# Kernel tuning notes

Hardware: AMD Instinct MI355X
Metric: run time of the kernel (lower is better)

Reference implementation:

```python
import jax, jax.numpy as jnp
import numpy as np

D = 1024
H = 16
HD = D // H
MLP = 4 * D
EPS = 1e-6
SCALE = HD ** -0.5


def _p(key, shape, s=0.02):
    return jax.random.normal(key, shape, dtype=jnp.float32) * s


def setup_inputs() -> dict:
    key = jax.random.key(0)
    ks = jax.random.split(key, 24)
    B, N, S = 4, 1024, 77
    return {
        "x": jax.random.normal(ks[0], (B, N, D), dtype=jnp.float32),
        "t_emb": jax.random.normal(ks[1], (B, D), dtype=jnp.float32),
        "context": jax.random.normal(ks[2], (B, S, D), dtype=jnp.float32),
        # AdaLN modulation: SiLU -> Linear(D, 6D)
        "adaln_w": _p(ks[3], (D, 6 * D)),
        "adaln_b": _p(ks[4], (6 * D,)),
        # self-attention
        "qkv_w": _p(ks[5], (D, 3 * D)),
        "qkv_b": _p(ks[6], (3 * D,)),
        "sa_proj_w": _p(ks[7], (D, D)),
        "sa_proj_b": _p(ks[8], (D,)),
        # cross-attention
        "q_w": _p(ks[9], (D, D)),
        "q_b": _p(ks[10], (D,)),
        "kv_w": _p(ks[11], (D, 2 * D)),
        "kv_b": _p(ks[12], (2 * D,)),
        "ca_proj_w": _p(ks[13], (D, D)),
        "ca_proj_b": _p(ks[14], (D,)),
        # MLP (GELU tanh)
        "fc1_w": _p(ks[15], (D, MLP)),
        "fc1_b": _p(ks[16], (MLP,)),
        "fc2_w": _p(ks[17], (MLP, D)),
        "fc2_b": _p(ks[18], (D,)),
    }


def _ln(x):
    # LayerNorm, elementwise_affine=False, eps=1e-6
    mu = jnp.mean(x, axis=-1, keepdims=True)
    var = jnp.var(x, axis=-1, keepdims=True)
    return (x - mu) * jax.lax.rsqrt(var + EPS)


def _heads(t):
    # [B, L, D] -> [B, H, L, HD]
    B, L, _ = t.shape
    return t.reshape(B, L, H, HD).transpose(0, 2, 1, 3)


def _attend(q, k, v):
    # q: [B,H,N,HD], k/v: [B,H,S,HD]
    attn = jnp.einsum("bhnd,bhsd->bhns", q, k) * SCALE
    attn = jax.nn.softmax(attn, axis=-1)
    o = jnp.einsum("bhns,bhsd->bhnd", attn, v)
    B, _, N, _ = q.shape
    return o.transpose(0, 2, 1, 3).reshape(B, N, D)


def reference(x, t_emb, context,
              adaln_w, adaln_b,
              qkv_w, qkv_b, sa_proj_w, sa_proj_b,
              q_w, q_b, kv_w, kv_b, ca_proj_w, ca_proj_b,
              fc1_w, fc1_b, fc2_w, fc2_b):
    B, N, _ = x.shape
    S = context.shape[1]

    # AdaLN modulation params
    mod = jax.nn.silu(t_emb) @ adaln_w + adaln_b            # [B, 6D]
    sh_sa, sc_sa, g_sa, sh_ff, sc_ff, g_ff = jnp.split(mod[:, None, :], 6, axis=-1)

    # --- self-attention branch ---
    xm = _ln(x) * (1.0 + sc_sa) + sh_sa
    qkv = (xm @ qkv_w + qkv_b).reshape(B, N, 3, H, HD)
    q = qkv[:, :, 0].transpose(0, 2, 1, 3)
    k = qkv[:, :, 1].transpose(0, 2, 1, 3)
    v = qkv[:, :, 2].transpose(0, 2, 1, 3)
    x_sa = _attend(q, k, v) @ sa_proj_w + sa_proj_b
    x = x + g_sa * x_sa

    # --- cross-attention branch ---
    xn = _ln(x)
    q = _heads(xn @ q_w + q_b)
    kv = (context @ kv_w + kv_b).reshape(B, S, 2, H, HD)
    k = kv[:, :, 0].transpose(0, 2, 1, 3)
    v = kv[:, :, 1].transpose(0, 2, 1, 3)
    x_ca = _attend(q, k, v) @ ca_proj_w + ca_proj_b
    x = x + x_ca

    # --- MLP branch ---
    xm = _ln(x) * (1.0 + sc_ff) + sh_ff
    h = jax.nn.gelu(xm @ fc1_w + fc1_b, approximate=True)
    x_ff = h @ fc2_w + fc2_b
    x = x + g_ff * x_ff
    return x
```

## Files before the change

kernel.cpp:

```cpp
#include <hip/hip_runtime.h>
#include <hip/hip_bf16.h>


#define D_MODEL 1024
#define NHEAD   16
#define HDIM    64
#define SEQ_N   1024
#define SEQ_S   77
#define BATCH   4
#define MLP_DIM 4096
#define ATT_SCALE 0.125f

typedef _Float16 f16;
typedef f16   f16x8 __attribute__((ext_vector_type(8)));
typedef float f32x4 __attribute__((ext_vector_type(4)));

__device__ __forceinline__ void gload16(const void* g, void* l) {
  __builtin_amdgcn_global_load_lds(
      (const __attribute__((address_space(1))) void*)g,
      (__attribute__((address_space(3))) void*)l, 16, 0, 0);
}

__global__ __launch_bounds__(256) void wt_kernel(
    const float* __restrict__ W, f16* __restrict__ Wt, int K, int N)
{
  __shared__ f16 tile[64][72];
  const int t = threadIdx.x;
  const int k0 = blockIdx.y * 64, n0 = blockIdx.x * 64;
  const int kr = t >> 4, nc = (t & 15) * 4;
#pragma unroll
  for (int p = 0; p < 4; ++p) {
    f32x4 v = *(const f32x4*)&W[(size_t)(k0 + kr + p * 16) * N + n0 + nc];
#pragma unroll
    for (int j = 0; j < 4; ++j) tile[nc + j][kr + p * 16] = (f16)v[j];
  }
  __syncthreads();
  const int nr = t >> 2, ck = (t & 3) * 16;
  *(f16x8*)&Wt[(size_t)(n0 + nr) * K + k0 + ck]     = *(const f16x8*)&tile[nr][ck];
  *(f16x8*)&Wt[(size_t)(n0 + nr) * K + k0 + ck + 8] = *(const f16x8*)&tile[nr][ck + 8];
}

__global__ __launch_bounds__(256) void mod_kernel(
    const float* __restrict__ t_emb, const float* __restrict__ w,
    const float* __restrict__ bias, float* __restrict__ mod)
{
  __shared__ float s[D_MODEL];
  const int b = blockIdx.y;
  for (int i = threadIdx.x; i < D_MODEL; i += 256) {
    float v = t_emb[b * D_MODEL + i];
    s[i] = v / (1.f + expf(-v));
  }
  __syncthreads();
  const int col = blockIdx.x * 256 + threadIdx.x;
  float acc = 0.f;
  for (int k = 0; k < D_MODEL; ++k) acc += s[k] * w[(size_t)k * (6 * D_MODEL) + col];
  mod[(size_t)b * (6 * D_MODEL) + col] = acc + bias[col];
}

__global__ __launch_bounds__(256) void init_x_kernel(
    const float* __restrict__ x, float* __restrict__ X, int n)
{
  int i = blockIdx.x * 256 + threadIdx.x;
  if (i < n) X[i] = x[i];
}

__global__ __launch_bounds__(256) void cvt_kernel(
    const float* __restrict__ in, f16* __restrict__ out, int n)
{
  int i = blockIdx.x * 256 + threadIdx.x;
  if (i < n) out[i] = (f16)in[i];
}

__global__ __launch_bounds__(256) void lnmod_kernel(
    const float* __restrict__ X, const float* __restrict__ mod,
    int scale_off, int shift_off, f16* __restrict__ out)
{
  const int row = blockIdx.x;
  const int b = row >> 10;
  const float* xr = X + (size_t)row * D_MODEL;
  float s = 0.f, s2 = 0.f;
  for (int i = threadIdx.x; i < D_MODEL; i += 256) {
    float v = xr[i]; s += v; s2 += v * v;
  }
  const int lane = threadIdx.x & 63, w = threadIdx.x >> 6;
  for (int o = 32; o; o >>= 1) { s += __shfl_xor(s, o); s2 += __shfl_xor(s2, o); }
  __shared__ float rs[4], rs2[4];
  if (lane == 0) { rs[w] = s; rs2[w] = s2; }
  __syncthreads();
  s = rs[0] + rs[1] + rs[2] + rs[3];
  s2 = rs2[0] + rs2[1] + rs2[2] + rs2[3];
  const float mean = s * (1.f / D_MODEL);
  const float var = s2 * (1.f / D_MODEL) - mean * mean;
  const float rstd = rsqrtf(var + 1e-6f);
  const float* mrow = mod ? mod + (size_t)b * (6 * D_MODEL) : nullptr;
  for (int i = threadIdx.x; i < D_MODEL; i += 256) {
    float v = (xr[i] - mean) * rstd;
    if (mrow) v = v * (1.f + mrow[scale_off + i]) + mrow[shift_off + i];
    out[(size_t)row * D_MODEL + i] = (f16)v;
  }
}

template <int BN>
__global__ __launch_bounds__(256) void gemm_kernel(
    const f16* __restrict__ A, const f16* __restrict__ Wt,
    const float* __restrict__ bias,
    float* __restrict__ Xres, const float* __restrict__ gate,
    f16* __restrict__ outb, float* __restrict__ outf,
    int M, int N, int K, int do_gelu)
{
  constexpr int NB = BN / 32;
  __shared__ f16 As[3][128 * 32];
  __shared__ f16 Bs[3][BN * 32];
  const int t = threadIdx.x;
  const int lane = t & 63, wave = t >> 6;
  const int wr = wave >> 1, wc = wave & 1;
  int bx = blockIdx.x, by = blockIdx.y;
  {
    const int gx = gridDim.x;
    const int nwg = gx * gridDim.y;
    if ((nwg & 7) == 0) {
      int wg = by * gx + bx;
      wg = (wg & 7) * (nwg >> 3) + (wg >> 3);
      bx = wg % gx; by = wg / gx;
    }
  }
  const int brow = by * 128, bcol = bx * BN;
  const int fr = lane & 15, fq = lane >> 4;
  const int sr = t >> 2, sc = (t & 3) * 8;
  const int ldsoff = wave * 512;

  f32x4 acc[4][NB] = {};
  const f16* Ag = A  + (size_t)(brow + sr) * K + sc;
  const f16* Bg = Wt + (size_t)(bcol + sr) * K + sc;
  const int nt = K >> 5;

  auto STAGE = [&](int buf, int k0) {
    gload16(Ag + k0,                  &As[buf][ldsoff]);
    gload16(Ag + (size_t)64 * K + k0, &As[buf][2048 + ldsoff]);
    gload16(Bg + k0,                  &Bs[buf][ldsoff]);
    if constexpr (BN == 128)
      gload16(Bg + (size_t)64 * K + k0, &Bs[buf][2048 + ldsoff]);
  };

  STAGE(0, 0);
  if (nt > 1) STAGE(1, 32);
  int cur = 0;
  for (int kt = 0; kt < nt; ++kt) {
    if constexpr (BN == 128)
      asm volatile("s_waitcnt vmcnt(4)\n\ts_barrier" ::: "memory");
    else
      asm volatile("s_waitcnt vmcnt(3)\n\ts_barrier" ::: "memory");
    int nx = cur + 2; if (nx >= 3) nx -= 3;
    if (kt + 2 < nt) STAGE(nx, (kt + 2) * 32);
    f16x8 af[4], bf[NB];
#pragma unroll
    for (int m = 0; m < 4; ++m)
      af[m] = *(const f16x8*)&As[cur][(wr * 64 + m * 16 + fr) * 32 + fq * 8];
#pragma unroll
    for (int n = 0; n < NB; ++n)
      bf[n] = *(const f16x8*)&Bs[cur][(wc * (BN / 2) + n * 16 + fr) * 32 + fq * 8];
#pragma unroll
    for (int m = 0; m < 4; ++m)
#pragma unroll
      for (int n = 0; n < NB; ++n)
        acc[m][n] = __builtin_amdgcn_mfma_f32_16x16x32_f16(af[m], bf[n], acc[m][n], 0, 0, 0);
    ++cur; if (cur == 3) cur = 0;
  }

#pragma unroll
  for (int m = 0; m < 4; ++m) {
#pragma unroll
    for (int n = 0; n < NB; ++n) {
      const int col = bcol + wc * (BN / 2) + n * 16 + fr;
      const int row0 = brow + wr * 64 + m * 16 + fq * 4;
      const float bv = bias ? bias[col] : 0.f;
#pragma unroll
      for (int r = 0; r < 4; ++r) {
        const int row = row0 + r;
        if (row >= M) continue;
        float v = acc[m][n][r] + bv;
        if (do_gelu) {
          float u = v;
          v = 0.5f * u * (1.f + tanhf(0.7978845608028654f * (u + 0.044715f * u * u * u)));
        }
        if (Xres) {
          const float g = gate ? gate[(size_t)(row >> 10) * (6 * D_MODEL) + col] : 1.0f;
          v = Xres[(size_t)row * N + col] + g * v;
          Xres[(size_t)row * N + col] = v;
        }
        if (outb) outb[(size_t)row * N + col] = (f16)v;
        if (outf) outf[(size_t)row * N + col] = v;
      }
    }
  }
}

__global__ __launch_bounds__(256) void sa_attn_kernel(
    const f16* __restrict__ qkv, f16* __restrict__ out)
{
  const int qt = blockIdx.x, h = blockIdx.y, b = blockIdx.z;
  __shared__ f16 Kl[64][72];
  __shared__ f16 Vt[64][72];
  __shared__ f16 Pl[4][16][72];
  const int t = threadIdx.x;
  const int lane = t & 63, w = t >> 6;
  const int fr = lane & 15, fq = lane >> 4;
  const size_t base = (size_t)b * SEQ_N * 3072 + h * 64;

  const int qrow = qt * 64 + w * 16 + fr;
  f16x8 qa[2];
#pragma unroll
  for (int kk = 0; kk < 2; ++kk)
    qa[kk] = *(const f16x8*)&qkv[base + (size_t)qrow * 3072 + kk * 32 + fq * 8];

  f32x4 o_acc[4] = {};
  float m_run[4], l_run[4];
#pragma unroll
  for (int r = 0; r < 4; ++r) { m_run[r] = -1e30f; l_run[r] = 0.f; }

  const int sr = t >> 2, scol = (t & 3) * 8;
  for (int s0 = 0; s0 < SEQ_N; s0 += 64) {
    __syncthreads();
#pragma unroll
    for (int p = 0; p < 2; ++p) {
      *(f16x8*)&Kl[sr][scol + p * 32] =
          *(const f16x8*)&qkv[base + (size_t)(s0 + sr) * 3072 + 1024 + scol + p * 32];
      f16x8 v = *(const f16x8*)&qkv[base + (size_t)(s0 + sr) * 3072 + 2048 + scol + p * 32];
#pragma unroll
      for (int j = 0; j < 8; ++j) Vt[scol + p * 32 + j][sr] = v[j];
    }
    __syncthreads();

    f32x4 sf[4] = {};
#pragma unroll
    for (int kk = 0; kk < 2; ++kk) {
#pragma unroll
      for (int n = 0; n < 4; ++n) {
        f16x8 kb = *(const f16x8*)&Kl[n * 16 + fr][kk * 32 + fq * 8];
        sf[n] = __builtin_amdgcn_mfma_f32_16x16x32_f16(qa[kk], kb, sf[n], 0, 0, 0);
      }
    }

#pragma unroll
    for (int r = 0; r < 4; ++r) {
      float v = fmaxf(fmaxf(sf[0][r], sf[1][r]), fmaxf(sf[2][r], sf[3][r]));
#pragma unroll
      for (int o = 1; o < 16; o <<= 1) v = fmaxf(v, __shfl_xor(v, o));
      const float mn = fmaxf(m_run[r], v * ATT_SCALE);
      const float f = __builtin_expf(m_run[r] - mn);
      m_run[r] = mn;
#pragma unroll
      for (int n = 0; n < 4; ++n) o_acc[n][r] *= f;
      float rs = 0.f;
#pragma unroll
      for (int n = 0; n < 4; ++n) {
        float p = __builtin_expf(sf[n][r] * ATT_SCALE - mn);
        sf[n][r] = p;
        rs += p;
      }
#pragma unroll
      for (int o = 1; o < 16; o <<= 1) rs += __shfl_xor(rs, o);
      l_run[r] = l_run[r] * f + rs;
    }

#pragma unroll
    for (int n = 0; n < 4; ++n)
#pragma unroll
      for (int r = 0; r < 4; ++r)
        Pl[w][fq * 4 + r][n * 16 + fr] = (f16)sf[n][r];

#pragma unroll
    for (int kk = 0; kk < 2; ++kk) {
      f16x8 pa = *(const f16x8*)&Pl[w][fr][kk * 32 + fq * 8];
#pragma unroll
      for (int n = 0; n < 4; ++n) {
        f16x8 vb = *(const f16x8*)&Vt[n * 16 + fr][kk * 32 + fq * 8];
        o_acc[n] = __builtin_amdgcn_mfma_f32_16x16x32_f16(pa, vb, o_acc[n], 0, 0, 0);
      }
    }
  }

  const size_t orow = (size_t)(b * SEQ_N + qt * 64 + w * 16) * D_MODEL + h * 64;
#pragma unroll
  for (int r = 0; r < 4; ++r) {
    const float inv = 1.f / l_run[r];
#pragma unroll
    for (int n = 0; n < 4; ++n)
      out[orow + (size_t)(fq * 4 + r) * D_MODEL + n * 16 + fr] = (f16)(o_acc[n][r] * inv);
  }
}

__global__ __launch_bounds__(256) void ca_attn_kernel(
    const f16* __restrict__ qb, const f16* __restrict__ kvb,
    f16* __restrict__ out)
{
  const int qt = blockIdx.x, h = blockIdx.y, b = blockIdx.z;
  __shared__ float qs[16][68];
  __shared__ float sc[16][80];
  __shared__ f16 kt[77][72];
  __shared__ f16 vt[77][72];
  const int t = threadIdx.x;
  for (int i = t; i < 16 * 64; i += 256) {
    int q = i >> 6, d = i & 63;
    qs[q][d] = (float)qb[(size_t)(b * SEQ_N + qt * 16 + q) * D_MODEL + h * 64 + d];
  }
  for (int i = t; i < SEQ_S * 8; i += 256) {
    int r = i >> 3, c = (i & 7) * 8;
    *(f16x8*)&kt[r][c] = *(const f16x8*)&kvb[(size_t)(b * SEQ_S + r) * 2048 + h * 64 + c];
    *(f16x8*)&vt[r][c] = *(const f16x8*)&kvb[(size_t)(b * SEQ_S + r) * 2048 + 1024 + h * 64 + c];
  }
  __syncthreads();
  for (int idx = t; idx < 16 * 80; idx += 256) {
    int q = idx / 80, s = idx % 80;
    float a = -1e30f;
    if (s < SEQ_S) {
      a = 0.f;
      for (int d = 0; d < 64; ++d) a += qs[q][d] * (float)kt[s][d];
      a *= ATT_SCALE;
    }
    sc[q][s] = a;
  }
  __syncthreads();
  const int lane = t & 63, w = t >> 6;
  for (int q = w; q < 16; q += 4) {
    float m = -1e30f;
    for (int j = lane; j < 80; j += 64) m = fmaxf(m, sc[q][j]);
    for (int o = 32; o; o >>= 1) m = fmaxf(m, __shfl_xor(m, o));
    float sum = 0.f;
    for (int j = lane; j < 80; j += 64) {
      float e = (j < SEQ_S) ? expf(sc[q][j] - m) : 0.f;
      sc[q][j] = e; sum += e;
    }
    for (int o = 32; o; o >>= 1) sum += __shfl_xor(sum, o);
    float inv = 1.f / sum;
    for (int j = lane; j < 80; j += 64) sc[q][j] *= inv;
  }
  __syncthreads();
  const int q = t >> 4, d0 = (t & 15) * 4;
  float a0 = 0, a1 = 0, a2 = 0, a3 = 0;
  for (int s = 0; s < SEQ_S; ++s) {
    float p = sc[q][s];
    a0 += p * (float)vt[s][d0];
    a1 += p * (float)vt[s][d0 + 1];
    a2 += p * (float)vt[s][d0 + 2];
    a3 += p * (float)vt[s][d0 + 3];
  }
  size_t orow = (size_t)(b * SEQ_N + qt * 16 + q) * D_MODEL + h * 64;
  out[orow + d0] = (f16)a0;
  out[orow + d0 + 1] = (f16)a1;
  out[orow + d0 + 2] = (f16)a2;
  out[orow + d0 + 3] = (f16)a3;
}

extern "C" void kernel_launch(void* const* d_in, const int* in_sizes, int n_in,
                              void* d_out, int out_size, void* d_ws, size_t ws_size,
                              hipStream_t stream)
{
  const float* x       = (const float*)d_in[0];
  const float* t_emb   = (const float*)d_in[1];
  const float* ctx     = (const float*)d_in[2];
  const float* adaln_w = (const float*)d_in[3];
  const float* adaln_b = (const float*)d_in[4];
  const float* qkv_w   = (const float*)d_in[5];
  const float* qkv_b   = (const float*)d_in[6];
  const float* sa_pw   = (const float*)d_in[7];
  const float* sa_pb   = (const float*)d_in[8];
  const float* q_w     = (const float*)d_in[9];
  const float* q_b     = (const float*)d_in[10];
  const float* kv_w    = (const float*)d_in[11];
  const float* kv_b    = (const float*)d_in[12];
  const float* ca_pw   = (const float*)d_in[13];
  const float* ca_pb   = (const float*)d_in[14];
  const float* fc1_w   = (const float*)d_in[15];
  const float* fc1_b   = (const float*)d_in[16];
  const float* fc2_w   = (const float*)d_in[17];
  const float* fc2_b   = (const float*)d_in[18];
  float* out = (float*)d_out;

  char* ws = (char*)d_ws;
  float* mod    = (float*)(ws + 0);
  float* X      = (float*)(ws + 98304);
  f16*   bufA   = (f16*)(ws + 16875520);
  f16*   bufB   = (f16*)(ws + 25264128);
  f16*   bufC   = (f16*)(ws + 50429952);
  f16*   bufKV  = (f16*)(ws + 58818560);
  f16*   ctxh   = (f16*)(ws + 60080128);
  f16*   qkv_wt = (f16*)(ws + 60866560);
  f16*   kv_wt  = (f16*)(ws + 67158016);
  f16*   sa_pwt = (f16*)(ws + 71352320);
  f16*   q_wt   = (f16*)(ws + 73449472);
  f16*   ca_pwt = (f16*)(ws + 75546624);
  f16*   fc1_wt = (f16*)(ws + 77643776);
  f16*   fc2_wt = (f16*)(ws + 86032384);
  f16*   bufQ   = bufB;

  const dim3 blk(256);
  const int TOK = BATCH * SEQ_N;
  const int CTX_ELE = BATCH * SEQ_S * D_MODEL;

  wt_kernel<<<dim3(48, 16), blk, 0, stream>>>(qkv_w, qkv_wt, 1024, 3072);
  wt_kernel<<<dim3(32, 16), blk, 0, stream>>>(kv_w,  kv_wt,  1024, 2048);
  wt_kernel<<<dim3(16, 16), blk, 0, stream>>>(sa_pw, sa_pwt, 1024, 1024);
  wt_kernel<<<dim3(16, 16), blk, 0, stream>>>(q_w,   q_wt,   1024, 1024);
  wt_kernel<<<dim3(16, 16), blk, 0, stream>>>(ca_pw, ca_pwt, 1024, 1024);
  wt_kernel<<<dim3(64, 16), blk, 0, stream>>>(fc1_w, fc1_wt, 1024, 4096);
  wt_kernel<<<dim3(16, 64), blk, 0, stream>>>(fc2_w, fc2_wt, 4096, 1024);

  mod_kernel<<<dim3(24, BATCH), blk, 0, stream>>>(t_emb, adaln_w, adaln_b, mod);
  init_x_kernel<<<dim3(TOK * D_MODEL / 256), blk, 0, stream>>>(x, X, TOK * D_MODEL);
  cvt_kernel<<<dim3((CTX_ELE + 255) / 256), blk, 0, stream>>>(ctx, ctxh, CTX_ELE);

  lnmod_kernel<<<TOK, blk, 0, stream>>>(X, mod, 1024, 0, bufA);
  gemm_kernel<128><<<dim3(3072 / 128, TOK / 128), blk, 0, stream>>>(
      bufA, qkv_wt, qkv_b, nullptr, nullptr, bufB, nullptr, TOK, 3072, 1024, 0);
  gemm_kernel<64><<<dim3(2048 / 64, 3), blk, 0, stream>>>(
      ctxh, kv_wt, kv_b, nullptr, nullptr, bufKV, nullptr, BATCH * SEQ_S, 2048, 1024, 0);
  sa_attn_kernel<<<dim3(SEQ_N / 64, NHEAD, BATCH), blk, 0, stream>>>(bufB, bufC);
  gemm_kernel<64><<<dim3(1024 / 64, TOK / 128), blk, 0, stream>>>(
      bufC, sa_pwt, sa_pb, X, mod + 2048, nullptr, nullptr, TOK, 1024, 1024, 0);

  lnmod_kernel<<<TOK, blk, 0, stream>>>(X, nullptr, 0, 0, bufA);
  gemm_kernel<64><<<dim3(1024 / 64, TOK / 128), blk, 0, stream>>>(
      bufA, q_wt, q_b, nullptr, nullptr, bufQ, nullptr, TOK, 1024, 1024, 0);
  ca_attn_kernel<<<dim3(SEQ_N / 16, NHEAD, BATCH), blk, 0, stream>>>(bufQ, bufKV, bufC);
  gemm_kernel<64><<<dim3(1024 / 64, TOK / 128), blk, 0, stream>>>(
      bufC, ca_pwt, ca_pb, X, nullptr, nullptr, nullptr, TOK, 1024, 1024, 0);

  lnmod_kernel<<<TOK, blk, 0, stream>>>(X, mod, 4096, 3072, bufA);
  gemm_kernel<128><<<dim3(MLP_DIM / 128, TOK / 128), blk, 0, stream>>>(
      bufA, fc1_wt, fc1_b, nullptr, nullptr, bufB, nullptr, TOK, MLP_DIM, 1024, 1);
  gemm_kernel<64><<<dim3(1024 / 64, TOK / 128), blk, 0, stream>>>(
      bufB, fc2_wt, fc2_b, X, mod + 5120, nullptr, out, TOK, 1024, MLP_DIM, 0);
}
```

Measured before the change: 551.1 us.

## Prefetch K/V into registers and use exp2 softmax with deferred row-sum reduction

The self-attention kernel now loads the next K/V tile into registers right after the barrier, so global loads overlap with the MFMA and softmax work, and the V transpose mapping is changed to reduce LDS conflicts. The scale times log2(e) is folded into Q up front so the softmax uses exp2 without a per-element multiply. The per-tile row-sum shuffle reduction is moved to a single reduction at the end. The cross-attention softmax also switches to exp2. Rounding the pre-scaled Q to fp16 slightly changes precision.

```diff
diff --git a/kernel.cpp b/kernel.cpp
--- a/kernel.cpp
+++ b/kernel.cpp
@@ -10,6 +10,7 @@
 #define BATCH   4
 #define MLP_DIM 4096
 #define ATT_SCALE 0.125f
+#define LOG2E_SCALE 0.1803368801111f
 
 typedef _Float16 f16;
 typedef f16   f16x8 __attribute__((ext_vector_type(8)));
@@ -210,26 +211,41 @@
   const int qrow = qt * 64 + w * 16 + fr;
   f16x8 qa[2];
 #pragma unroll
-  for (int kk = 0; kk < 2; ++kk)
+  for (int kk = 0; kk < 2; ++kk) {
     qa[kk] = *(const f16x8*)&qkv[base + (size_t)qrow * 3072 + kk * 32 + fq * 8];
+#pragma unroll
+    for (int j = 0; j < 8; ++j)
+      qa[kk][j] = (f16)((float)qa[kk][j] * LOG2E_SCALE);
+  }
 
   f32x4 o_acc[4] = {};
   float m_run[4], l_run[4];
 #pragma unroll
   for (int r = 0; r < 4; ++r) { m_run[r] = -1e30f; l_run[r] = 0.f; }
 
-  const int sr = t >> 2, scol = (t & 3) * 8;
+  const int ksr = t >> 2, ksc = (t & 3) * 8;
+  const int vs = t & 63, vd = (t >> 6) * 16;
+  f16x8 kreg0, kreg1, vreg0, vreg1;
+
+  auto LOADKV = [&](int s0) {
+    kreg0 = *(const f16x8*)&qkv[base + (size_t)(s0 + ksr) * 3072 + 1024 + ksc];
+    kreg1 = *(const f16x8*)&qkv[base + (size_t)(s0 + ksr) * 3072 + 1024 + ksc + 32];
+    vreg0 = *(const f16x8*)&qkv[base + (size_t)(s0 + vs) * 3072 + 2048 + vd];
+    vreg1 = *(const f16x8*)&qkv[base + (size_t)(s0 + vs) * 3072 + 2048 + vd + 8];
+  };
+
+  LOADKV(0);
   for (int s0 = 0; s0 < SEQ_N; s0 += 64) {
     __syncthreads();
-#pragma unroll
-    for (int p = 0; p < 2; ++p) {
-      *(f16x8*)&Kl[sr][scol + p * 32] =
-          *(const f16x8*)&qkv[base + (size_t)(s0 + sr) * 3072 + 1024 + scol + p * 32];
-      f16x8 v = *(const f16x8*)&qkv[base + (size_t)(s0 + sr) * 3072 + 2048 + scol + p * 32];
-#pragma unroll
-      for (int j = 0; j < 8; ++j) Vt[scol + p * 32 + j][sr] = v[j];
+    *(f16x8*)&Kl[ksr][ksc]      = kreg0;
+    *(f16x8*)&Kl[ksr][ksc + 32] = kreg1;
+#pragma unroll
+    for (int j = 0; j < 8; ++j) {
+      Vt[vd + j][vs]     = vreg0[j];
+      Vt[vd + 8 + j][vs] = vreg1[j];
     }
     __syncthreads();
+    if (s0 + 64 < SEQ_N) LOADKV(s0 + 64);
 
     f32x4 sf[4] = {};
 #pragma unroll
@@ -246,20 +262,18 @@
       float v = fmaxf(fmaxf(sf[0][r], sf[1][r]), fmaxf(sf[2][r], sf[3][r]));
 #pragma unroll
       for (int o = 1; o < 16; o <<= 1) v = fmaxf(v, __shfl_xor(v, o));
-      const float mn = fmaxf(m_run[r], v * ATT_SCALE);
-      const float f = __builtin_expf(m_run[r] - mn);
+      const float mn = fmaxf(m_run[r], v);
+      const float f = exp2f(m_run[r] - mn);
       m_run[r] = mn;
 #pragma unroll
       for (int n = 0; n < 4; ++n) o_acc[n][r] *= f;
       float rs = 0.f;
 #pragma unroll
       for (int n = 0; n < 4; ++n) {
-        float p = __builtin_expf(sf[n][r] * ATT_SCALE - mn);
+        float p = exp2f(sf[n][r] - mn);
         sf[n][r] = p;
         rs += p;
       }
-#pragma unroll
-      for (int o = 1; o < 16; o <<= 1) rs += __shfl_xor(rs, o);
       l_run[r] = l_run[r] * f + rs;
     }
 
@@ -283,7 +297,10 @@
   const size_t orow = (size_t)(b * SEQ_N + qt * 64 + w * 16) * D_MODEL + h * 64;
 #pragma unroll
   for (int r = 0; r < 4; ++r) {
-    const float inv = 1.f / l_run[r];
+    float l = l_run[r];
+#pragma unroll
+    for (int o = 1; o < 16; o <<= 1) l += __shfl_xor(l, o);
+    const float inv = 1.f / l;
 #pragma unroll
     for (int n = 0; n < 4; ++n)
       out[orow + (size_t)(fq * 4 + r) * D_MODEL + n * 16 + fr] = (f16)(o_acc[n][r] * inv);
@@ -316,7 +333,7 @@
     if (s < SEQ_S) {
       a = 0.f;
       for (int d = 0; d < 64; ++d) a += qs[q][d] * (float)kt[s][d];
-      a *= ATT_SCALE;
+      a *= LOG2E_SCALE;
     }
     sc[q][s] = a;
   }
@@ -328,7 +345,7 @@
     for (int o = 32; o; o >>= 1) m = fmaxf(m, __shfl_xor(m, o));
     float sum = 0.f;
     for (int j = lane; j < 80; j += 64) {
-      float e = (j < SEQ_S) ? expf(sc[q][j] - m) : 0.f;
+      float e = (j < SEQ_S) ? exp2f(sc[q][j] - m) : 0.f;
       sc[q][j] = e; sum += e;
     }
     for (int o = 32; o; o >>= 1) sum += __shfl_xor(sum, o);
```

After: 523.3 us. 1.05x faster.
